# Performance work log

Hardware: AMD Instinct MI355X
Metric: run time of the kernel (lower is better)

Reference implementation:

```python
import jax, jax.numpy as jnp
from jax import lax
import numpy as np

D = 1024      # input_size
H = D // 2    # proj hidden
T = 25        # num_ner_labels
B, S = 64, 512


def setup_inputs() -> dict:
    key = jax.random.key(0)
    ks = jax.random.split(key, 8)
    sc1 = 1.0 / np.sqrt(D)
    sc2 = 1.0 / np.sqrt(H)
    return {
        "encoder_out": jax.random.normal(ks[0], (B, S, D), dtype=jnp.float32),
        "W1": jax.random.uniform(ks[1], (D, H), jnp.float32, -sc1, sc1),
        "b1": jax.random.uniform(ks[2], (H,), jnp.float32, -sc1, sc1),
        "W2": jax.random.uniform(ks[3], (H, T), jnp.float32, -sc2, sc2),
        "b2": jax.random.uniform(ks[4], (T,), jnp.float32, -sc2, sc2),
        "start_trans": jax.random.uniform(ks[5], (T,), jnp.float32, -0.1, 0.1),
        "end_trans": jax.random.uniform(ks[6], (T,), jnp.float32, -0.1, 0.1),
        "trans": jax.random.uniform(ks[7], (T, T), jnp.float32, -0.1, 0.1),
        "ner_labels": jax.random.randint(jax.random.fold_in(key, 1), (B, S), 0, T, dtype=jnp.int64),
        "mask": jnp.ones((B, S), dtype=bool),
    }


def _crf_nll(emissions, start_trans, end_trans, trans, labels, mask):
    # torchcrf negative mean log-likelihood, batch_first
    maskf = mask.astype(emissions.dtype)
    # numerator: score of gold path
    em_at_tag = jnp.take_along_axis(emissions, labels[..., None], axis=2)[..., 0]  # [B,S]
    score0 = start_trans[labels[:, 0]] + em_at_tag[:, 0]
    trans_sc = trans[labels[:, :-1], labels[:, 1:]]                                # [B,S-1]
    step_score = (trans_sc + em_at_tag[:, 1:]) * maskf[:, 1:]
    last_idx = mask.sum(axis=1).astype(jnp.int32) - 1
    last_tag = jnp.take_along_axis(labels, last_idx[:, None].astype(labels.dtype), axis=1)[:, 0]
    numerator = score0 + step_score.sum(axis=1) + end_trans[last_tag]
    # denominator: log partition via forward algorithm (scan over time)
    alpha0 = start_trans[None, :] + emissions[:, 0]                                # [B,T]
    em_rest = jnp.swapaxes(emissions[:, 1:], 0, 1)                                 # [S-1,B,T]
    m_rest = jnp.swapaxes(mask[:, 1:], 0, 1)                                       # [S-1,B]

    def step(alpha, xs):
        em_t, m_t = xs
        new = jax.scipy.special.logsumexp(
            alpha[:, :, None] + trans[None, :, :] + em_t[:, None, :], axis=1)
        return jnp.where(m_t[:, None], new, alpha), None

    alpha, _ = lax.scan(step, alpha0, (em_rest, m_rest))
    log_Z = jax.scipy.special.logsumexp(alpha + end_trans[None, :], axis=1)        # [B]
    return -jnp.mean(numerator - log_Z)


def reference(encoder_out, W1, b1, W2, b2, start_trans, end_trans, trans, ner_labels, mask):
    h = jax.nn.gelu(encoder_out @ W1 + b1, approximate=False)  # dropout is eval-mode identity
    emissions = h @ W2 + b2                                    # [B,S,T]
    return _crf_nll(emissions, start_trans, end_trans, trans, ner_labels, mask)
```

## Files before the change

### kernel.cpp

```cpp
#include <hip/hip_runtime.h>
#include <math.h>

#define DD 1024
#define HH 512
#define TT 25
#define BB 64
#define SS 512
#define MM (BB*SS)
#define NC 32
#define EMPL ((size_t)MM * TT)

typedef __attribute__((ext_vector_type(8))) short short8;
typedef __attribute__((ext_vector_type(4))) float floatx4;
typedef __attribute__((ext_vector_type(16))) float floatx16;

static __device__ __forceinline__ unsigned short f2bf(float f) {
  unsigned u = __float_as_uint(f);
  u = (u + 0x7FFFu + ((u >> 16) & 1u)) >> 16;
  return (unsigned short)u;
}
static __device__ __forceinline__ float rl(float v, int i) {
  return __int_as_float(__builtin_amdgcn_readlane(__float_as_int(v), i));
}
static __device__ __forceinline__ void load_lds16(const void* g, void* l) {
  __builtin_amdgcn_global_load_lds(
      (const __attribute__((address_space(1))) unsigned int*)g,
      (__attribute__((address_space(3))) unsigned int*)l, 16, 0, 0);
}
union U4S8 { uint4 u; short8 s; };

__global__ __launch_bounds__(256) void k_prep(
    const float* __restrict__ W1, const float* __restrict__ W2,
    unsigned short* __restrict__ W1T2, unsigned short* __restrict__ W2p,
    unsigned* __restrict__ cnt) {
  const int t = threadIdx.x;
  if (blockIdx.y < 8) {
    __shared__ unsigned short tile[64 * 72];
    const int k0 = blockIdx.x * 64, n0 = blockIdx.y * 64;
    #pragma unroll
    for (int it = 0; it < 16; it++) {
      int idx = t + it * 256;
      int kk = idx >> 6, nn = idx & 63;
      tile[nn * 72 + kk] = f2bf(W1[(size_t)(k0 + kk) * HH + n0 + nn]);
    }
    __syncthreads();
    #pragma unroll
    for (int it = 0; it < 4; it++) {
      int idx = (t + it * 256) * 4;
      int nn = idx >> 6, kk = idx & 63;
      ushort4 v;
      v.x = tile[nn * 72 + kk];     v.y = tile[nn * 72 + kk + 1];
      v.z = tile[nn * 72 + kk + 2]; v.w = tile[nn * 72 + kk + 3];
      int kt = (k0 >> 5) + (kk >> 5), kkk = kk & 31;
      int n = n0 + nn;
      size_t slice = (size_t)kt * (HH * 32) + (size_t)(n & ~63) * 32;
      int o = ((((n & 63) * 64) + ((kkk >> 3) * 16)) ^ ((n & 7) << 4)) + (kkk & 7) * 2;
      *(ushort4*)((char*)W1T2 + slice * 2 + o) = v;
    }
  } else {
    if (blockIdx.x == 0 && t == 0) *cnt = 0u;
    #pragma unroll
    for (int e = 0; e < 4; e++) {
      int idx = blockIdx.x * 1024 + t + e * 256;
      int row = idx >> 9, k = idx & 511;
      float v = (row < TT) ? W2[(size_t)k * TT + row] : 0.f;
      W2p[(size_t)row * HH + k] = f2bf(v);
    }
  }
}

__global__ __launch_bounds__(256, 4) void k_emis(
    const float* __restrict__ X, const unsigned short* __restrict__ W1T2,
    const float* __restrict__ b1, const unsigned short* __restrict__ W2p,
    const float* __restrict__ b2, float* __restrict__ em) {
  __shared__ __attribute__((aligned(16))) short lds[18432];

  const int tid  = threadIdx.x;
  const int lane = tid & 63;
  const int w    = tid >> 6;
  const int l15  = lane & 15;
  const int kc   = lane >> 4;
  const int yb   = blockIdx.y;
  const int m0   = blockIdx.x * 64;
  const int colbase = yb * 256;

  floatx4 acc[4][4];
  #pragma unroll
  for (int a = 0; a < 4; a++)
    #pragma unroll
    for (int b = 0; b < 4; b++)
      acc[a][b] = (floatx4){0.f, 0.f, 0.f, 0.f};

  const int am = tid >> 2;
  const int ac = tid & 3;
  const float* Xrow = X + (size_t)(m0 + am) * DD + ac * 8;
  const int xwb = (am * 64 + ac * 16) ^ ((am & 7) << 4);

  const unsigned short* gW = W1T2 + (size_t)(colbase + w * 64) * 32 + lane * 8;

  {
    short* lW = lds + 2048 + w * 2048;
    #pragma unroll
    for (int j = 0; j < 4; j++)
      load_lds16(gW + j * 512, lW + j * 512);
  }
  float4 xa0 = *(const float4*)(Xrow);
  float4 xa1 = *(const float4*)(Xrow + 4);
  float4 xb0 = *(const float4*)(Xrow + 32);
  float4 xb1 = *(const float4*)(Xrow + 36);

  for (int t = 0; t < 32; ++t) {
    short* sBc = lds + 2048 + (t & 1) * 8192;

    float4 xc0, xc1;
    if (t < 31) {
      short* lW = lds + 2048 + ((t + 1) & 1) * 8192 + w * 2048;
      const unsigned short* g = gW + (size_t)(t + 1) * (HH * 32);
      #pragma unroll
      for (int j = 0; j < 4; j++)
        load_lds16(g + j * 512, lW + j * 512);
    }
    if (t < 30) {
      xc0 = *(const float4*)(Xrow + (t + 2) * 32);
      xc1 = *(const float4*)(Xrow + (t + 2) * 32 + 4);
    }

    {
      unsigned p0 = (unsigned)f2bf(xa0.x) | ((unsigned)f2bf(xa0.y) << 16);
      unsigned p1 = (unsigned)f2bf(xa0.z) | ((unsigned)f2bf(xa0.w) << 16);
      unsigned p2 = (unsigned)f2bf(xa1.x) | ((unsigned)f2bf(xa1.y) << 16);
      unsigned p3 = (unsigned)f2bf(xa1.z) | ((unsigned)f2bf(xa1.w) << 16);
      *(uint4*)((char*)lds + xwb) = make_uint4(p0, p1, p2, p3);
    }
    xa0 = xb0; xa1 = xb1;
    if (t < 30) { xb0 = xc0; xb1 = xc1; }

    if (t < 31) {
      asm volatile("s_waitcnt vmcnt(6) lgkmcnt(0)" ::: "memory");
    } else {
      asm volatile("s_waitcnt vmcnt(0) lgkmcnt(0)" ::: "memory");
    }
    __builtin_amdgcn_s_barrier();
    asm volatile("" ::: "memory");

    short8 af[4], bfr[4];
    #pragma unroll
    for (int mt = 0; mt < 4; mt++) {
      int row = mt * 16 + l15;
      af[mt] = *(const short8*)((char*)lds + ((row * 64 + kc * 16) ^ ((l15 & 7) << 4)));
    }
    #pragma unroll
    for (int nt = 0; nt < 4; nt++) {
      int rloc = nt * 16 + l15;
      int off = (rloc * 64 + kc * 16) ^ ((l15 & 7) << 4);
      bfr[nt] = *(const short8*)((char*)(sBc + w * 2048) + off);
    }
    asm volatile("s_waitcnt lgkmcnt(0)" ::: "memory");
    __builtin_amdgcn_sched_barrier(0);
    #pragma unroll
    for (int mt = 0; mt < 4; mt++)
      #pragma unroll
      for (int nt = 0; nt < 4; nt++)
        acc[mt][nt] = __builtin_amdgcn_mfma_f32_16x16x32_bf16(af[mt], bfr[nt], acc[mt][nt], 0, 0, 0);

    asm volatile("" ::: "memory");
    __builtin_amdgcn_s_barrier();
    asm volatile("" ::: "memory");
  }

  short* sH = lds;
  float* sC = (float*)(lds + 8448);
  const int mt_g = w & 1, kh_g = w >> 1;
  float* emp = em + (size_t)yb * EMPL;

  short8 w2f[2][4];
  #pragma unroll
  for (int nt2 = 0; nt2 < 2; nt2++)
    #pragma unroll
    for (int ks = 0; ks < 4; ks++)
      w2f[nt2][ks] = *(const short8*)(W2p + (size_t)(nt2 * 16 + l15) * HH
                                      + colbase + kh_g * 128 + ks * 32 + kc * 8);

  #pragma unroll
  for (int half = 0; half < 2; half++) {
    __syncthreads();
    #pragma unroll
    for (int mt2 = 0; mt2 < 2; mt2++) {
      int mt = half * 2 + mt2;
      #pragma unroll
      for (int nt = 0; nt < 4; nt++) {
        int n = w * 64 + nt * 16 + l15;
        float bias = b1[colbase + n];
        #pragma unroll
        for (int r = 0; r < 4; r++) {
          int ml = mt2 * 16 + kc * 4 + r;
          float v = acc[mt][nt][r] + bias;
          float g = 0.5f * v * (1.0f + erff(v * 0.70710678118654752f));
          sH[ml * 264 + n] = (short)f2bf(g);
        }
      }
    }
    __syncthreads();
    #pragma unroll
    for (int nt2 = 0; nt2 < 2; nt2++) {
      floatx4 c2 = (floatx4){0.f, 0.f, 0.f, 0.f};
      #pragma unroll
      for (int ks = 0; ks < 4; ks++) {
        short8 a2 = *(const short8*)(sH + (mt_g * 16 + l15) * 264 + kh_g * 128 + ks * 32 + kc * 8);
        c2 = __builtin_amdgcn_mfma_f32_16x16x32_bf16(a2, w2f[nt2][ks], c2, 0, 0, 0);
      }
      #pragma unroll
      for (int r = 0; r < 4; r++)
        sC[kh_g * 1024 + (mt_g * 16 + kc * 4 + r) * 32 + nt2 * 16 + l15] = c2[r];
    }
    __syncthreads();
    for (int o = tid; o < 32 * TT; o += 256) {
      int m = o / TT, t = o % TT;
      float val = sC[m * 32 + t] + sC[1024 + m * 32 + t];
      if (yb == 0) val += b2[t];
      emp[(size_t)(m0 + half * 32 + m) * TT + t] = val;
    }
  }
}

__global__ __launch_bounds__(256) void k_chunk(
    const float* __restrict__ em, const float* __restrict__ trans,
    float* __restrict__ Mats) {
  const int b = blockIdx.x;
  const int c = blockIdx.y * 4 + (threadIdx.x >> 6);
  const int lane = threadIdx.x & 63;
  const int h = lane >> 5;
  const int n = lane & 31;
  const float* e0 = em + (size_t)b * SS * TT;
  const float* e1 = e0 + EMPL;

  unsigned a1p[4], a2p[4];
  #pragma unroll
  for (int p = 0; p < 4; p++) {
    int i0 = h * 8 + 2 * p, i1 = i0 + 1;
    unsigned lo = (n < TT && i0 < TT) ? (unsigned)f2bf(__expf(trans[i0 * TT + n])) : 0u;
    unsigned hi = (n < TT && i1 < TT) ? (unsigned)f2bf(__expf(trans[i1 * TT + n])) : 0u;
    a1p[p] = lo | (hi << 16);
    int j0 = 16 + h * 8 + 2 * p, j1 = j0 + 1;
    lo = (n < TT && j0 < TT) ? (unsigned)f2bf(__expf(trans[j0 * TT + n])) : 0u;
    hi = (n < TT && j1 < TT) ? (unsigned)f2bf(__expf(trans[j1 * TT + n])) : 0u;
    a2p[p] = lo | (hi << 16);
  }
  U4S8 A1, A2;
  A1.u = make_uint4(a1p[0], a1p[1], a1p[2], a1p[3]);
  A2.u = make_uint4(a2p[0], a2p[1], a2p[2], a2p[3]);

  unsigned bp1[4], bp2[4];
  #pragma unroll
  for (int p = 0; p < 4; p++) {
    int k0 = h * 8 + 2 * p;
    bp1[p] = ((k0 == n) ? 0x3F80u : 0u) | ((k0 + 1 == n) ? 0x3F800000u : 0u);
    int k2 = 16 + h * 8 + 2 * p;
    bp2[p] = ((k2 == n) ? 0x3F80u : 0u) | ((k2 + 1 == n) ? 0x3F800000u : 0u);
  }

  const int s0 = 1 + c * 16;
  const int nst = (s0 + 16 <= SS) ? 16 : (SS - s0);

  float emv[16], f[16];
  #pragma unroll
  for (int e = 0; e < 16; e++) {
    int r = (e & 3) + 8 * (e >> 2) + 4 * h;
    emv[e] = (r < TT) ? (e0[s0 * TT + r] + e1[s0 * TT + r]) : 0.f;
  }

  for (int t = 0; t < nst; t++) {
    const float rs = (t == 8) ? 32.0f : 0.0f;
    float ex[16];
    #pragma unroll
    for (int e = 0; e < 16; e++) ex[e] = __expf(emv[e] - rs);
    int sn = (s0 + t + 1 < SS) ? s0 + t + 1 : SS - 1;
    #pragma unroll
    for (int e = 0; e < 16; e++) {
      int r = (e & 3) + 8 * (e >> 2) + 4 * h;
      emv[e] = (r < TT) ? (e0[sn * TT + r] + e1[sn * TT + r]) : 0.f;
    }
    U4S8 B1, B2;
    B1.u = make_uint4(bp1[0], bp1[1], bp1[2], bp1[3]);
    B2.u = make_uint4(bp2[0], bp2[1], bp2[2], bp2[3]);
    floatx16 D = __builtin_amdgcn_mfma_f32_32x32x16_bf16(A1.s, B1.s,
                   __builtin_amdgcn_mfma_f32_32x32x16_bf16(A2.s, B2.s,
                     (floatx16){0.f,0.f,0.f,0.f,0.f,0.f,0.f,0.f,
                                0.f,0.f,0.f,0.f,0.f,0.f,0.f,0.f}, 0,0,0), 0,0,0);
    #pragma unroll
    for (int e = 0; e < 16; e++) f[e] = D[e] * ex[e];
    if (t == nst - 1) break;
    unsigned P[16];
    #pragma unroll
    for (int p = 0; p < 8; p++)
      P[p] = (unsigned)f2bf(f[2 * p]) | ((unsigned)f2bf(f[2 * p + 1]) << 16);
    unsigned sp[8];
    #pragma unroll
    for (int p = 0; p < 8; p++)
      sp[p] = (unsigned)__shfl_xor((int)P[p], 32);
    bool up = (h == 1);
    bp1[0] = up ? sp[2] : P[0];
    bp1[1] = up ? sp[3] : P[1];
    bp1[2] = up ? P[2] : sp[0];
    bp1[3] = up ? P[3] : sp[1];
    bp2[0] = up ? sp[6] : P[4];
    bp2[1] = up ? sp[7] : P[5];
    bp2[2] = up ? P[6] : sp[4];
    bp2[3] = up ? P[7] : sp[5];
  }

  if (n < TT) {
    float* Mc = Mats + ((size_t)(b * NC + c)) * (TT * TT) + n * TT;
    #pragma unroll
    for (int e = 0; e < 16; e++) {
      int r = (e & 3) + 8 * (e >> 2) + 4 * h;
      if (r < TT) Mc[r] = __logf(f[e]) + 32.0f;
    }
  }
}

static __device__ __forceinline__ float foldchunk(
    const float* col, float a, int tid) {
  float mxc = -1e30f;
  #pragma unroll
  for (int i = 0; i < TT; i++) mxc = fmaxf(mxc, col[i]);
  float a0 = __builtin_amdgcn_readfirstlane(a);
  float p = __expf(a - a0);
  float d0 = 0.f, d1 = 0.f, d2 = 0.f, d3 = 0.f;
  #pragma unroll
  for (int i = 0; i < 24; i += 4) {
    d0 = fmaf(rl(p, i + 0), __expf(col[i + 0] - mxc), d0);
    d1 = fmaf(rl(p, i + 1), __expf(col[i + 1] - mxc), d1);
    d2 = fmaf(rl(p, i + 2), __expf(col[i + 2] - mxc), d2);
    d3 = fmaf(rl(p, i + 3), __expf(col[i + 3] - mxc), d3);
  }
  d0 = fmaf(rl(p, 24), __expf(col[24] - mxc), d0);
  float anew = a0 + mxc + __logf((d0 + d1) + (d2 + d3));
  return (tid < TT) ? anew : -1e30f;
}

__global__ __launch_bounds__(64) void k_comb(
    const float* __restrict__ em, const float* __restrict__ start,
    const float* __restrict__ endt, const float* __restrict__ trans,
    const int* __restrict__ labels, const float* __restrict__ Mats,
    float* __restrict__ partial, unsigned* __restrict__ cnt,
    float* __restrict__ out) {
  const int b = blockIdx.x;
  const int tid = threadIdx.x;
  const float* e0 = em + (size_t)b * SS * TT;
  const float* e1 = e0 + EMPL;
  const int* lab = labels + b * SS;

  float part = 0.f;
  for (int s = tid; s < SS; s += 64) {
    int l = lab[s];
    if (s == 0) part += start[l] + (e0[l] + e1[l]);
    else        part += trans[lab[s - 1] * TT + l] + (e0[s * TT + l] + e1[s * TT + l]);
  }
  #pragma unroll
  for (int off = 32; off; off >>= 1) part += __shfl_xor(part, off);
  float num = part + endt[lab[SS - 1]];

  const int jj = (tid < TT) ? tid : 0;
  float a = (tid < TT) ? start[tid] + (e0[tid] + e1[tid]) : -1e30f;
  const float* Mb = Mats + (size_t)b * NC * (TT * TT);

  float cA[TT], cB[TT];
  #pragma unroll
  for (int i = 0; i < TT; i++) cA[i] = Mb[i * TT + jj];
  for (int c = 0; c < NC; c += 2) {
    const float* M1 = Mb + (size_t)(c + 1) * (TT * TT);
    #pragma unroll
    for (int i = 0; i < TT; i++) cB[i] = M1[i * TT + jj];
    a = foldchunk(cA, a, tid);
    if (c + 2 < NC) {
      const float* M2 = Mb + (size_t)(c + 2) * (TT * TT);
      #pragma unroll
      for (int i = 0; i < TT; i++) cA[i] = M2[i * TT + jj];
    }
    a = foldchunk(cB, a, tid);
  }

  float v = (tid < TT) ? a + endt[tid] : -1e30f;
  float mx = v;
  #pragma unroll
  for (int off = 16; off; off >>= 1) mx = fmaxf(mx, __shfl_xor(mx, off, 32));
  float e = (tid < TT) ? __expf(v - mx) : 0.f;
  #pragma unroll
  for (int off = 16; off; off >>= 1) e += __shfl_xor(e, off, 32);
  if (tid == 0) partial[b] = (mx + __logf(e)) - num;

  __threadfence();
  __shared__ unsigned ticket;
  if (tid == 0)
    ticket = __hip_atomic_fetch_add(cnt, 1u, __ATOMIC_ACQ_REL,
                                    __HIP_MEMORY_SCOPE_AGENT);
  __syncthreads();
  if (ticket == BB - 1) {
    __threadfence();
    float s = partial[tid];
    #pragma unroll
    for (int off = 32; off; off >>= 1) s += __shfl_xor(s, off);
    if (tid == 0) out[0] = s * (1.0f / 64.0f);
  }
}

extern "C" void kernel_launch(void* const* d_in, const int* in_sizes, int n_in,
                              void* d_out, int out_size, void* d_ws, size_t ws_size,
                              hipStream_t stream) {
  const float* X   = (const float*)d_in[0];
  const float* W1  = (const float*)d_in[1];
  const float* b1  = (const float*)d_in[2];
  const float* W2  = (const float*)d_in[3];
  const float* b2  = (const float*)d_in[4];
  const float* st  = (const float*)d_in[5];
  const float* en  = (const float*)d_in[6];
  const float* tr  = (const float*)d_in[7];
  const int* labels = (const int*)d_in[8];

  char* ws = (char*)d_ws;
  unsigned short* W1T2 = (unsigned short*)ws;
  unsigned short* W2p  = (unsigned short*)(ws + 0x100000);
  float* em            = (float*)(ws + 0x110000);
  float* Mats          = (float*)(ws + 0x750000);
  float* partial       = (float*)(ws + 0xC40000);
  unsigned* cnt        = (unsigned*)(ws + 0xC40100);

  k_prep <<<dim3(16, 9), 256, 0, stream>>>(W1, W2, W1T2, W2p, cnt);
  k_emis <<<dim3(512, 2), 256, 0, stream>>>(X, W1T2, b1, W2p, b2, em);
  k_chunk<<<dim3(BB, 8), 256, 0, stream>>>(em, tr, Mats);
  k_comb <<<BB, 64, 0, stream>>>(em, st, en, tr, labels, Mats, partial, cnt,
                                 (float*)d_out);
}
```

Baseline: 300.1 us.

## Fuse CRF combine step into chunk kernel via per-batch atomic tickets

Merges the k_comb kernel into k_chunk. The last of the 8 blocks for each batch row, found with a per-batch atomic counter, performs the sequential chunk fold and numerator computation. A second global counter picks the final block that reduces the mean. This removes one kernel launch and its gap, at the cost of atomics and fences in every chunk block and per-batch folds that now start whenever each batch row finishes.

Measured after the change: 386.4 us. 1.29x slower.

```diff
diff --git a/kernel.cpp b/kernel.cpp
--- a/kernel.cpp
+++ b/kernel.cpp
@@ -32,7 +32,7 @@
 __global__ __launch_bounds__(256) void k_prep(
     const float* __restrict__ W1, const float* __restrict__ W2,
     unsigned short* __restrict__ W1T2, unsigned short* __restrict__ W2p,
-    unsigned* __restrict__ cnt) {
+    unsigned* __restrict__ cntb) {
   const int t = threadIdx.x;
   if (blockIdx.y < 8) {
     __shared__ unsigned short tile[64 * 72];
@@ -58,7 +58,7 @@
       *(ushort4*)((char*)W1T2 + slice * 2 + o) = v;
     }
   } else {
-    if (blockIdx.x == 0 && t == 0) *cnt = 0u;
+    if (blockIdx.x == 0 && t < 65) cntb[t] = 0u;
     #pragma unroll
     for (int e = 0; e < 4; e++) {
       int idx = blockIdx.x * 1024 + t + e * 256;
@@ -223,9 +223,32 @@
   }
 }
 
+static __device__ __forceinline__ float foldchunk(
+    const float* col, float a, int tid) {
+  float mxc = -1e30f;
+  #pragma unroll
+  for (int i = 0; i < TT; i++) mxc = fmaxf(mxc, col[i]);
+  float a0 = __builtin_amdgcn_readfirstlane(a);
+  float p = __expf(a - a0);
+  float d0 = 0.f, d1 = 0.f, d2 = 0.f, d3 = 0.f;
+  #pragma unroll
+  for (int i = 0; i < 24; i += 4) {
+    d0 = fmaf(rl(p, i + 0), __expf(col[i + 0] - mxc), d0);
+    d1 = fmaf(rl(p, i + 1), __expf(col[i + 1] - mxc), d1);
+    d2 = fmaf(rl(p, i + 2), __expf(col[i + 2] - mxc), d2);
+    d3 = fmaf(rl(p, i + 3), __expf(col[i + 3] - mxc), d3);
+  }
+  d0 = fmaf(rl(p, 24), __expf(col[24] - mxc), d0);
+  float anew = a0 + mxc + __logf((d0 + d1) + (d2 + d3));
+  return (tid < TT) ? anew : -1e30f;
+}
+
 __global__ __launch_bounds__(256) void k_chunk(
     const float* __restrict__ em, const float* __restrict__ trans,
-    float* __restrict__ Mats) {
+    float* __restrict__ Mats, const float* __restrict__ start,
+    const float* __restrict__ endt, const int* __restrict__ labels,
+    float* __restrict__ partial, unsigned* __restrict__ cntb,
+    float* __restrict__ out) {
   const int b = blockIdx.x;
   const int c = blockIdx.y * 4 + (threadIdx.x >> 6);
   const int lane = threadIdx.x & 63;
@@ -317,91 +340,70 @@
       if (r < TT) Mc[r] = __logf(f[e]) + 32.0f;
     }
   }
-}
-
-static __device__ __forceinline__ float foldchunk(
-    const float* col, float a, int tid) {
-  float mxc = -1e30f;
-  #pragma unroll
-  for (int i = 0; i < TT; i++) mxc = fmaxf(mxc, col[i]);
-  float a0 = __builtin_amdgcn_readfirstlane(a);
-  float p = __expf(a - a0);
-  float d0 = 0.f, d1 = 0.f, d2 = 0.f, d3 = 0.f;
-  #pragma unroll
-  for (int i = 0; i < 24; i += 4) {
-    d0 = fmaf(rl(p, i + 0), __expf(col[i + 0] - mxc), d0);
-    d1 = fmaf(rl(p, i + 1), __expf(col[i + 1] - mxc), d1);
-    d2 = fmaf(rl(p, i + 2), __expf(col[i + 2] - mxc), d2);
-    d3 = fmaf(rl(p, i + 3), __expf(col[i + 3] - mxc), d3);
-  }
-  d0 = fmaf(rl(p, 24), __expf(col[24] - mxc), d0);
-  float anew = a0 + mxc + __logf((d0 + d1) + (d2 + d3));
-  return (tid < TT) ? anew : -1e30f;
-}
-
-__global__ __launch_bounds__(64) void k_comb(
-    const float* __restrict__ em, const float* __restrict__ start,
-    const float* __restrict__ endt, const float* __restrict__ trans,
-    const int* __restrict__ labels, const float* __restrict__ Mats,
-    float* __restrict__ partial, unsigned* __restrict__ cnt,
-    float* __restrict__ out) {
-  const int b = blockIdx.x;
-  const int tid = threadIdx.x;
-  const float* e0 = em + (size_t)b * SS * TT;
-  const float* e1 = e0 + EMPL;
-  const int* lab = labels + b * SS;
-
-  float part = 0.f;
-  for (int s = tid; s < SS; s += 64) {
-    int l = lab[s];
-    if (s == 0) part += start[l] + (e0[l] + e1[l]);
-    else        part += trans[lab[s - 1] * TT + l] + (e0[s * TT + l] + e1[s * TT + l]);
-  }
-  #pragma unroll
-  for (int off = 32; off; off >>= 1) part += __shfl_xor(part, off);
-  float num = part + endt[lab[SS - 1]];
-
-  const int jj = (tid < TT) ? tid : 0;
-  float a = (tid < TT) ? start[tid] + (e0[tid] + e1[tid]) : -1e30f;
-  const float* Mb = Mats + (size_t)b * NC * (TT * TT);
-
-  float cA[TT], cB[TT];
-  #pragma unroll
-  for (int i = 0; i < TT; i++) cA[i] = Mb[i * TT + jj];
-  for (int c = 0; c < NC; c += 2) {
-    const float* M1 = Mb + (size_t)(c + 1) * (TT * TT);
-    #pragma unroll
-    for (int i = 0; i < TT; i++) cB[i] = M1[i * TT + jj];
-    a = foldchunk(cA, a, tid);
-    if (c + 2 < NC) {
-      const float* M2 = Mb + (size_t)(c + 2) * (TT * TT);
-      #pragma unroll
-      for (int i = 0; i < TT; i++) cA[i] = M2[i * TT + jj];
-    }
-    a = foldchunk(cB, a, tid);
-  }
-
-  float v = (tid < TT) ? a + endt[tid] : -1e30f;
-  float mx = v;
-  #pragma unroll
-  for (int off = 16; off; off >>= 1) mx = fmaxf(mx, __shfl_xor(mx, off, 32));
-  float e = (tid < TT) ? __expf(v - mx) : 0.f;
-  #pragma unroll
-  for (int off = 16; off; off >>= 1) e += __shfl_xor(e, off, 32);
-  if (tid == 0) partial[b] = (mx + __logf(e)) - num;
 
   __threadfence();
-  __shared__ unsigned ticket;
-  if (tid == 0)
-    ticket = __hip_atomic_fetch_add(cnt, 1u, __ATOMIC_ACQ_REL,
-                                    __HIP_MEMORY_SCOPE_AGENT);
+  __shared__ unsigned tk;
+  if (threadIdx.x == 0)
+    tk = __hip_atomic_fetch_add(&cntb[b], 1u, __ATOMIC_ACQ_REL,
+                                __HIP_MEMORY_SCOPE_AGENT);
   __syncthreads();
-  if (ticket == BB - 1) {
+  if (tk == 7 && threadIdx.x < 64) {
     __threadfence();
-    float s = partial[tid];
-    #pragma unroll
-    for (int off = 32; off; off >>= 1) s += __shfl_xor(s, off);
-    if (tid == 0) out[0] = s * (1.0f / 64.0f);
+    const int tid = threadIdx.x;
+    const int* lab = labels + b * SS;
+
+    float part = 0.f;
+    for (int s = tid; s < SS; s += 64) {
+      int l = lab[s];
+      if (s == 0) part += start[l] + (e0[l] + e1[l]);
+      else        part += trans[lab[s - 1] * TT + l] + (e0[s * TT + l] + e1[s * TT + l]);
+    }
+    #pragma unroll
+    for (int off = 32; off; off >>= 1) part += __shfl_xor(part, off);
+    float num = part + endt[lab[SS - 1]];
+
+    const int jj = (tid < TT) ? tid : 0;
+    float a = (tid < TT) ? start[tid] + (e0[tid] + e1[tid]) : -1e30f;
+    const float* Mb = Mats + (size_t)b * NC * (TT * TT);
+
+    float cA[TT], cB[TT];
+    #pragma unroll
+    for (int i = 0; i < TT; i++) cA[i] = Mb[i * TT + jj];
+    for (int cc = 0; cc < NC; cc += 2) {
+      const float* M1 = Mb + (size_t)(cc + 1) * (TT * TT);
+      #pragma unroll
+      for (int i = 0; i < TT; i++) cB[i] = M1[i * TT + jj];
+      a = foldchunk(cA, a, tid);
+      if (cc + 2 < NC) {
+        const float* M2 = Mb + (size_t)(cc + 2) * (TT * TT);
+        #pragma unroll
+        for (int i = 0; i < TT; i++) cA[i] = M2[i * TT + jj];
+      }
+      a = foldchunk(cB, a, tid);
+    }
+
+    float v = (tid < TT) ? a + endt[tid] : -1e30f;
+    float mx = v;
+    #pragma unroll
+    for (int off = 16; off; off >>= 1) mx = fmaxf(mx, __shfl_xor(mx, off, 32));
+    float e = (tid < TT) ? __expf(v - mx) : 0.f;
+    #pragma unroll
+    for (int off = 16; off; off >>= 1) e += __shfl_xor(e, off, 32);
+    if (tid == 0) partial[b] = (mx + __logf(e)) - num;
+
+    __threadfence();
+    unsigned t2 = 0;
+    if (tid == 0)
+      t2 = __hip_atomic_fetch_add(&cntb[BB], 1u, __ATOMIC_ACQ_REL,
+                                  __HIP_MEMORY_SCOPE_AGENT);
+    t2 = (unsigned)__shfl((int)t2, 0);
+    if (t2 == BB - 1) {
+      __threadfence();
+      float s2 = partial[tid];
+      #pragma unroll
+      for (int off = 32; off; off >>= 1) s2 += __shfl_xor(s2, off);
+      if (tid == 0) out[0] = s2 * (1.0f / 64.0f);
+    }
   }
 }
 
@@ -424,11 +426,10 @@
   float* em            = (float*)(ws + 0x110000);
   float* Mats          = (float*)(ws + 0x750000);
   float* partial       = (float*)(ws + 0xC40000);
-  unsigned* cnt        = (unsigned*)(ws + 0xC40100);
-
-  k_prep <<<dim3(16, 9), 256, 0, stream>>>(W1, W2, W1T2, W2p, cnt);
+  unsigned* cntb       = (unsigned*)(ws + 0xC40100);
+
+  k_prep <<<dim3(16, 9), 256, 0, stream>>>(W1, W2, W1T2, W2p, cntb);
   k_emis <<<dim3(512, 2), 256, 0, stream>>>(X, W1T2, b1, W2p, b2, em);
-  k_chunk<<<dim3(BB, 8), 256, 0, stream>>>(em, tr, Mats);
-  k_comb <<<BB, 64, 0, stream>>>(em, st, en, tr, labels, Mats, partial, cnt,
-                                 (float*)d_out);
-}
+  k_chunk<<<dim3(BB, 8), 256, 0, stream>>>(em, tr, Mats, st, en, labels,
+                                           partial, cntb, (float*)d_out);
+}
```

## Pre-convert X to bf16 fragment layout and load MFMA A operands directly

Applied to the files above, without the earlier changes.

Adds a prep pass that converts the fp32 encoder output into bf16 stored in MFMA-fragment order, so the GEMM kernel loads A fragments straight into registers instead of converting and staging them through LDS each k-step. The main loop is unrolled by two with ping-pong W1 buffers and no per-step block barrier. It keeps a fallback kernel for small workspaces. The trade is an extra full pass over X (read fp32, write bf16) plus the re-read, while the X traffic is still read twice, once per column half.

Result: slower. 319.9 us (+6.6%).

```diff
diff --git a/kernel.cpp b/kernel.cpp
--- a/kernel.cpp
+++ b/kernel.cpp
@@ -30,13 +30,15 @@
 union U4S8 { uint4 u; short8 s; };
 
 __global__ __launch_bounds__(256) void k_prep(
-    const float* __restrict__ W1, const float* __restrict__ W2,
-    unsigned short* __restrict__ W1T2, unsigned short* __restrict__ W2p,
-    unsigned* __restrict__ cnt) {
+    const float* __restrict__ X, const float* __restrict__ W1,
+    const float* __restrict__ W2, unsigned short* __restrict__ W1T2,
+    unsigned short* __restrict__ W2p, unsigned short* __restrict__ Xf,
+    unsigned* __restrict__ cntb) {
   const int t = threadIdx.x;
-  if (blockIdx.y < 8) {
+  const int bid = blockIdx.x;
+  if (bid < 128) {
     __shared__ unsigned short tile[64 * 72];
-    const int k0 = blockIdx.x * 64, n0 = blockIdx.y * 64;
+    const int k0 = (bid & 15) * 64, n0 = (bid >> 4) * 64;
     #pragma unroll
     for (int it = 0; it < 16; it++) {
       int idx = t + it * 256;
@@ -57,23 +59,38 @@
       int o = ((((n & 63) * 64) + ((kkk >> 3) * 16)) ^ ((n & 7) << 4)) + (kkk & 7) * 2;
       *(ushort4*)((char*)W1T2 + slice * 2 + o) = v;
     }
-  } else {
-    if (blockIdx.x == 0 && t == 0) *cnt = 0u;
+  } else if (bid < 144) {
+    const int x = bid - 128;
+    if (x == 0 && t < 65) cntb[t] = 0u;
     #pragma unroll
     for (int e = 0; e < 4; e++) {
-      int idx = blockIdx.x * 1024 + t + e * 256;
+      int idx = x * 1024 + t + e * 256;
       int row = idx >> 9, k = idx & 511;
       float v = (row < TT) ? W2[(size_t)k * TT + row] : 0.f;
       W2p[(size_t)row * HH + k] = f2bf(v);
     }
+  } else {
+    const int fid = (bid - 144) * 256 + t;
+    const int lane = fid & 63, mt = (fid >> 6) & 3;
+    const int tt = (fid >> 8) & 31, mb = fid >> 13;
+    const int m = mb * 64 + mt * 16 + (lane & 15);
+    const int c0 = tt * 32 + ((lane >> 4) << 3);
+    const float* xp = X + (size_t)m * DD + c0;
+    float4 a = *(const float4*)xp;
+    float4 b = *(const float4*)(xp + 4);
+    unsigned p0 = (unsigned)f2bf(a.x) | ((unsigned)f2bf(a.y) << 16);
+    unsigned p1 = (unsigned)f2bf(a.z) | ((unsigned)f2bf(a.w) << 16);
+    unsigned p2 = (unsigned)f2bf(b.x) | ((unsigned)f2bf(b.y) << 16);
+    unsigned p3 = (unsigned)f2bf(b.z) | ((unsigned)f2bf(b.w) << 16);
+    *(uint4*)(Xf + (size_t)fid * 8) = make_uint4(p0, p1, p2, p3);
   }
 }
 
 __global__ __launch_bounds__(256, 4) void k_emis(
-    const float* __restrict__ X, const unsigned short* __restrict__ W1T2,
+    const unsigned short* __restrict__ Xf, const unsigned short* __restrict__ W1T2,
     const float* __restrict__ b1, const unsigned short* __restrict__ W2p,
     const float* __restrict__ b2, float* __restrict__ em) {
-  __shared__ __attribute__((aligned(16))) short lds[18432];
+  __shared__ __attribute__((aligned(16))) short lds[16640];
 
   const int tid  = threadIdx.x;
   const int lane = tid & 63;
@@ -91,6 +108,155 @@
     for (int b = 0; b < 4; b++)
       acc[a][b] = (floatx4){0.f, 0.f, 0.f, 0.f};
 
+  const unsigned short* gXf = Xf + (size_t)blockIdx.x * 32 * 2048 + lane * 8;
+  const unsigned short* gW  = W1T2 + (size_t)(colbase + w * 64) * 32 + lane * 8;
+
+  short8 afA[4], afB[4];
+  #pragma unroll
+  for (int mt = 0; mt < 4; mt++)
+    afA[mt] = *(const short8*)(gXf + mt * 512);
+  {
+    short* lW = lds + w * 2048;
+    #pragma unroll
+    for (int j = 0; j < 4; j++)
+      load_lds16(gW + j * 512, lW + j * 512);
+  }
+
+  for (int t = 0; t < 32; t += 2) {
+    {
+      #pragma unroll
+      for (int mt = 0; mt < 4; mt++)
+        afB[mt] = *(const short8*)(gXf + (t + 1) * 2048 + mt * 512);
+      short* lW = lds + 8192 + w * 2048;
+      const unsigned short* g = gW + (size_t)(t + 1) * (HH * 32);
+      #pragma unroll
+      for (int j = 0; j < 4; j++)
+        load_lds16(g + j * 512, lW + j * 512);
+      asm volatile("s_waitcnt vmcnt(8)" ::: "memory");
+
+      short8 bfr[4];
+      #pragma unroll
+      for (int nt = 0; nt < 4; nt++) {
+        int rloc = nt * 16 + l15;
+        int off = (rloc * 64 + kc * 16) ^ ((l15 & 7) << 4);
+        bfr[nt] = *(const short8*)((char*)(lds + w * 2048) + off);
+      }
+      asm volatile("s_waitcnt lgkmcnt(0)" ::: "memory");
+      __builtin_amdgcn_sched_barrier(0);
+      #pragma unroll
+      for (int mt = 0; mt < 4; mt++)
+        #pragma unroll
+        for (int nt = 0; nt < 4; nt++)
+          acc[mt][nt] = __builtin_amdgcn_mfma_f32_16x16x32_bf16(afA[mt], bfr[nt], acc[mt][nt], 0, 0, 0);
+    }
+    {
+      if (t + 2 < 32) {
+        #pragma unroll
+        for (int mt = 0; mt < 4; mt++)
+          afA[mt] = *(const short8*)(gXf + (t + 2) * 2048 + mt * 512);
+        short* lW = lds + w * 2048;
+        const unsigned short* g = gW + (size_t)(t + 2) * (HH * 32);
+        #pragma unroll
+        for (int j = 0; j < 4; j++)
+          load_lds16(g + j * 512, lW + j * 512);
+        asm volatile("s_waitcnt vmcnt(8)" ::: "memory");
+      } else {
+        asm volatile("s_waitcnt vmcnt(0)" ::: "memory");
+      }
+
+      short8 bfr[4];
+      #pragma unroll
+      for (int nt = 0; nt < 4; nt++) {
+        int rloc = nt * 16 + l15;
+        int off = (rloc * 64 + kc * 16) ^ ((l15 & 7) << 4);
+        bfr[nt] = *(const short8*)((char*)(lds + 8192 + w * 2048) + off);
+      }
+      asm volatile("s_waitcnt lgkmcnt(0)" ::: "memory");
+      __builtin_amdgcn_sched_barrier(0);
+      #pragma unroll
+      for (int mt = 0; mt < 4; mt++)
+        #pragma unroll
+        for (int nt = 0; nt < 4; nt++)
+          acc[mt][nt] = __builtin_amdgcn_mfma_f32_16x16x32_bf16(afB[mt], bfr[nt], acc[mt][nt], 0, 0, 0);
+    }
+  }
+
+  short* sH = lds;
+  float* sC = (float*)(lds + 8448);
+  const int mt_g = w & 1, kh_g = w >> 1;
+  float* emp = em + (size_t)yb * EMPL;
+
+  short8 w2f[2][4];
+  #pragma unroll
+  for (int nt2 = 0; nt2 < 2; nt2++)
+    #pragma unroll
+    for (int ks = 0; ks < 4; ks++)
+      w2f[nt2][ks] = *(const short8*)(W2p + (size_t)(nt2 * 16 + l15) * HH
+                                      + colbase + kh_g * 128 + ks * 32 + kc * 8);
+
+  #pragma unroll
+  for (int half = 0; half < 2; half++) {
+    __syncthreads();
+    #pragma unroll
+    for (int mt2 = 0; mt2 < 2; mt2++) {
+      int mt = half * 2 + mt2;
+      #pragma unroll
+      for (int nt = 0; nt < 4; nt++) {
+        int n = w * 64 + nt * 16 + l15;
+        float bias = b1[colbase + n];
+        #pragma unroll
+        for (int r = 0; r < 4; r++) {
+          int ml = mt2 * 16 + kc * 4 + r;
+          float v = acc[mt][nt][r] + bias;
+          float g = 0.5f * v * (1.0f + erff(v * 0.70710678118654752f));
+          sH[ml * 264 + n] = (short)f2bf(g);
+        }
+      }
+    }
+    __syncthreads();
+    #pragma unroll
+    for (int nt2 = 0; nt2 < 2; nt2++) {
+      floatx4 c2 = (floatx4){0.f, 0.f, 0.f, 0.f};
+      #pragma unroll
+      for (int ks = 0; ks < 4; ks++) {
+        short8 a2 = *(const short8*)(sH + (mt_g * 16 + l15) * 264 + kh_g * 128 + ks * 32 + kc * 8);
+        c2 = __builtin_amdgcn_mfma_f32_16x16x32_bf16(a2, w2f[nt2][ks], c2, 0, 0, 0);
+      }
+      #pragma unroll
+      for (int r = 0; r < 4; r++)
+        sC[kh_g * 1024 + (mt_g * 16 + kc * 4 + r) * 32 + nt2 * 16 + l15] = c2[r];
+    }
+    __syncthreads();
+    for (int o = tid; o < 32 * TT; o += 256) {
+      int m = o / TT, t = o % TT;
+      float val = sC[m * 32 + t] + sC[1024 + m * 32 + t];
+      if (yb == 0) val += b2[t];
+      emp[(size_t)(m0 + half * 32 + m) * TT + t] = val;
+    }
+  }
+}
+
+__global__ __launch_bounds__(256, 4) void k_emis_fb(
+    const float* __restrict__ X, const unsigned short* __restrict__ W1T2,
+    const float* __restrict__ b1, const unsigned short* __restrict__ W2p,
+    const float* __restrict__ b2, float* __restrict__ em) {
+  __shared__ __attribute__((aligned(16))) short lds[18432];
+  const int tid  = threadIdx.x;
+  const int lane = tid & 63;
+  const int w    = tid >> 6;
+  const int l15  = lane & 15;
+  const int kc   = lane >> 4;
+  const int yb   = blockIdx.y;
+  const int m0   = blockIdx.x * 64;
+  const int colbase = yb * 256;
+
+  floatx4 acc[4][4];
+  #pragma unroll
+  for (int a = 0; a < 4; a++)
+    #pragma unroll
+    for (int b = 0; b < 4; b++)
+      acc[a][b] = (floatx4){0.f, 0.f, 0.f, 0.f};
+
   const int am = tid >> 2;
   const int ac = tid & 3;
   const float* Xrow = X + (size_t)(m0 + am) * DD + ac * 8;
@@ -111,7 +277,6 @@
 
   for (int t = 0; t < 32; ++t) {
     short* sBc = lds + 2048 + (t & 1) * 8192;
-
     float4 xc0, xc1;
     if (t < 31) {
       short* lW = lds + 2048 + ((t + 1) & 1) * 8192 + w * 2048;
@@ -124,7 +289,6 @@
       xc0 = *(const float4*)(Xrow + (t + 2) * 32);
       xc1 = *(const float4*)(Xrow + (t + 2) * 32 + 4);
     }
-
     {
       unsigned p0 = (unsigned)f2bf(xa0.x) | ((unsigned)f2bf(xa0.y) << 16);
       unsigned p1 = (unsigned)f2bf(xa0.z) | ((unsigned)f2bf(xa0.w) << 16);
@@ -135,11 +299,8 @@
     xa0 = xb0; xa1 = xb1;
     if (t < 30) { xb0 = xc0; xb1 = xc1; }
 
-    if (t < 31) {
-      asm volatile("s_waitcnt vmcnt(6) lgkmcnt(0)" ::: "memory");
-    } else {
-      asm volatile("s_waitcnt vmcnt(0) lgkmcnt(0)" ::: "memory");
-    }
+    if (t < 31) asm volatile("s_waitcnt vmcnt(6) lgkmcnt(0)" ::: "memory");
+    else        asm volatile("s_waitcnt vmcnt(0) lgkmcnt(0)" ::: "memory");
     __builtin_amdgcn_s_barrier();
     asm volatile("" ::: "memory");
 
@@ -424,11 +585,19 @@
   float* em            = (float*)(ws + 0x110000);
   float* Mats          = (float*)(ws + 0x750000);
   float* partial       = (float*)(ws + 0xC40000);
-  unsigned* cnt        = (unsigned*)(ws + 0xC40100);
-
-  k_prep <<<dim3(16, 9), 256, 0, stream>>>(W1, W2, W1T2, W2p, cnt);
-  k_emis <<<dim3(512, 2), 256, 0, stream>>>(X, W1T2, b1, W2p, b2, em);
+  unsigned* cntb       = (unsigned*)(ws + 0xC40100);
+  unsigned short* Xf   = (unsigned short*)(ws + 0xD00000);
+
+  const bool big = ws_size >= (size_t)0x4D00000;
+
+  if (big) {
+    k_prep<<<144 + 16384, 256, 0, stream>>>(X, W1, W2, W1T2, W2p, Xf, cntb);
+    k_emis<<<dim3(512, 2), 256, 0, stream>>>(Xf, W1T2, b1, W2p, b2, em);
+  } else {
+    k_prep<<<144, 256, 0, stream>>>(X, W1, W2, W1T2, W2p, Xf, cntb);
+    k_emis_fb<<<dim3(512, 2), 256, 0, stream>>>(X, W1T2, b1, W2p, b2, em);
+  }
   k_chunk<<<dim3(BB, 8), 256, 0, stream>>>(em, tr, Mats);
-  k_comb <<<BB, 64, 0, stream>>>(em, st, en, tr, labels, Mats, partial, cnt,
+  k_comb <<<BB, 64, 0, stream>>>(em, st, en, tr, labels, Mats, partial, cntb,
                                  (float*)d_out);
 }
```
